# Kernel tuning notes

Hardware: AMD Instinct MI355X
Metric: run time of the kernel (lower is better)

Reference implementation:

```python
import jax, jax.numpy as jnp
import numpy as np

B, T, D = 16, 1024, 768
H = 12
HD = D // H
MLP = 3072


def _layernorm(x, g, b, eps=1e-5):
    mu = jnp.mean(x, axis=-1, keepdims=True)
    var = jnp.var(x, axis=-1, keepdims=True)
    return (x - mu) * jax.lax.rsqrt(var + eps) * g + b


def setup_inputs() -> dict:
    key = jax.random.key(0)
    ks = jax.random.split(key, 12)
    s_d = 1.0 / np.sqrt(D)
    s_m = 1.0 / np.sqrt(MLP)
    return {
        "x": jax.random.normal(ks[0], (B, T, D), dtype=jnp.float32),
        "Wq": jax.random.uniform(ks[1], (D, D), jnp.float32, -s_d, s_d),
        "bq": jnp.zeros((D,), jnp.float32),
        "Wk": jax.random.uniform(ks[2], (D, D), jnp.float32, -s_d, s_d),
        "bk": jnp.zeros((D,), jnp.float32),
        "Wv": jax.random.uniform(ks[3], (D, D), jnp.float32, -s_d, s_d),
        "bv": jnp.zeros((D,), jnp.float32),
        "Wo": jax.random.uniform(ks[4], (D, D), jnp.float32, -s_d, s_d),
        "bo": jnp.zeros((D,), jnp.float32),
        "ln1_g": jnp.ones((D,), jnp.float32),
        "ln1_b": jnp.zeros((D,), jnp.float32),
        "ln2_g": jnp.ones((D,), jnp.float32),
        "ln2_b": jnp.zeros((D,), jnp.float32),
        "W1": jax.random.uniform(ks[5], (D, MLP), jnp.float32, -s_d, s_d),
        "b1": jnp.zeros((MLP,), jnp.float32),
        "W2": jax.random.uniform(ks[6], (MLP, D), jnp.float32, -s_m, s_m),
        "b2": jnp.zeros((D,), jnp.float32),
    }


def reference(x, Wq, bq, Wk, bk, Wv, bv, Wo, bo, ln1_g, ln1_b, ln2_g, ln2_b, W1, b1, W2, b2):
    h = _layernorm(x, ln1_g, ln1_b)
    # QKV projections -> [B, H, T, HD]
    q = (h @ Wq + bq).reshape(B, T, H, HD).transpose(0, 2, 1, 3)
    k = (h @ Wk + bk).reshape(B, T, H, HD).transpose(0, 2, 1, 3)
    v = (h @ Wv + bv).reshape(B, T, H, HD).transpose(0, 2, 1, 3)
    # NOTE: original divides by sqrt(input_dim), not sqrt(head_dim)
    scores = jnp.einsum('bhtf,bhjf->bhtj', q, k) / jnp.sqrt(jnp.float32(D))
    score = jax.nn.softmax(scores, axis=-1)
    attn = jnp.einsum('bhij,bhjf->bihf', score, v)  # [B, T, H, HD]
    attn_out = attn.reshape(B, T, D) @ Wo + bo
    out = attn_out + x
    h2 = _layernorm(out, ln2_g, ln2_b)
    # MLP: Linear -> GELU -> Linear -> GELU (GELU after 2nd linear is in the source)
    m = jax.nn.gelu(h2 @ W1 + b1, approximate=False)
    m = jax.nn.gelu(m @ W2 + b2, approximate=False)
    return m + out
```

## Files before the change

kernel.cpp:

```cpp
#include <hip/hip_runtime.h>
#include <hip/hip_bf16.h>
#include <math.h>

#define D_MODEL 768
#define T_SEQ   1024
#define B_BATCH 16
#define MLP_DIM 3072
#define M_ROWS  (B_BATCH * T_SEQ)

typedef __attribute__((ext_vector_type(8))) __bf16          bf16x8;
typedef __attribute__((ext_vector_type(4))) __bf16          bf16x4;
typedef __attribute__((ext_vector_type(4))) float           f32x4;

__device__ __forceinline__ float bf2f(unsigned short u) {
  union { unsigned int u; float f; } w; w.u = ((unsigned int)u) << 16; return w.f;
}
__device__ __forceinline__ unsigned short f2bf(float f) {
  union { float f; unsigned int u; } w; w.f = f;
  unsigned int r = (w.u + 0x7fffu + ((w.u >> 16) & 1u)) >> 16;
  return (unsigned short)r;
}
__device__ __forceinline__ float gelu_f(float x) {
  return 0.5f * x * (1.0f + erff(x * 0.70710678118654752f));
}
__device__ __forceinline__ void gload16(const void* g, void* l) {
  __builtin_amdgcn_global_load_lds(
      (const __attribute__((address_space(1))) unsigned int*)g,
      (__attribute__((address_space(3))) unsigned int*)l, 16, 0, 0);
}

__global__ void wtr_k(const float* __restrict__ src,
                      unsigned short* __restrict__ dst, int R, int C) {
  __shared__ float t[32][33];
  const int c0 = blockIdx.x * 32, r0 = blockIdx.y * 32;
  const int tx = threadIdx.x, ty = threadIdx.y;
  #pragma unroll
  for (int j = 0; j < 32; j += 8)
    t[ty + j][tx] = src[(size_t)(r0 + ty + j) * C + (c0 + tx)];
  __syncthreads();
  #pragma unroll
  for (int j = 0; j < 32; j += 8)
    dst[(size_t)(c0 + ty + j) * R + (r0 + tx)] = f2bf(t[tx][ty + j]);
}

__global__ void bcat_k(const float* __restrict__ a, const float* __restrict__ b,
                       const float* __restrict__ c, float* __restrict__ o) {
  const int i = blockIdx.x * 256 + threadIdx.x;
  if (i < 768) { o[i] = a[i]; o[i + 768] = b[i]; o[i + 1536] = c[i]; }
}

template<int SRC_F32>
__global__ __launch_bounds__(256) void ln_k(const void* __restrict__ src,
    const float* __restrict__ g, const float* __restrict__ b,
    unsigned short* __restrict__ out) {
  const int row = blockIdx.x, tid = threadIdx.x;
  const size_t base = (size_t)row * D_MODEL;
  float v[3];
  #pragma unroll
  for (int i = 0; i < 3; ++i) {
    const int c = tid + (i << 8);
    v[i] = SRC_F32 ? ((const float*)src)[base + c]
                   : bf2f(((const unsigned short*)src)[base + c]);
  }
  float s  = v[0] + v[1] + v[2];
  float sq = v[0]*v[0] + v[1]*v[1] + v[2]*v[2];
  #pragma unroll
  for (int m = 32; m; m >>= 1) { s += __shfl_xor(s, m); sq += __shfl_xor(sq, m); }
  __shared__ float ps[4], pq[4];
  if ((tid & 63) == 0) { ps[tid >> 6] = s; pq[tid >> 6] = sq; }
  __syncthreads();
  s  = ps[0] + ps[1] + ps[2] + ps[3];
  sq = pq[0] + pq[1] + pq[2] + pq[3];
  const float mu  = s * (1.0f / 768.0f);
  const float var = sq * (1.0f / 768.0f) - mu * mu;
  const float inv = rsqrtf(var + 1e-5f);
  #pragma unroll
  for (int i = 0; i < 3; ++i) {
    const int c = tid + (i << 8);
    out[base + c] = f2bf((v[i] - mu) * inv * g[c] + b[c]);
  }
}

template<int EP>
__global__ __launch_bounds__(512) void gemm_k(
    const unsigned short* __restrict__ Au, const unsigned short* __restrict__ Btu,
    const float* __restrict__ bias, void* __restrict__ outv,
    const void* __restrict__ residv, void* __restrict__ aux,
    int M, int N, int K, int cgrp) {
  __shared__ __align__(16) __bf16 SMEM[2 * 32768];
  const __bf16* A  = (const __bf16*)Au;
  const __bf16* Bt = (const __bf16*)Btu;
  const int tid = threadIdx.x;
  const int lane = tid & 63, w = tid >> 6;
  const int wr = w >> 2, wc = w & 3;
  const int lr = lane & 15, lg = lane >> 4;
  const int gx = gridDim.x, gy = gridDim.y;
  const int bid = blockIdx.y * gx + blockIdx.x;
  const int xcd = bid & 7, idx = bid >> 3;
  const int rpx = gx >> 3;
  const int gsz = rpx * cgrp;
  const int grp = idx / gsz, rem = idx - grp * gsz;
  const int rb = rem / cgrp, cc2 = rem - rb * cgrp + grp * cgrp;
  const int brow = (xcd * rpx + rb) * 256;
  const int bcol = cc2 * 256;

  f32x4 acc[8][4];
  #pragma unroll
  for (int m = 0; m < 8; ++m)
    #pragma unroll
    for (int n = 0; n < 4; ++n) acc[m][n] = (f32x4){0.f, 0.f, 0.f, 0.f};

  const int rrs = lane >> 2;
  const int ccs = (lane & 3) << 3;
  const int csw = ccs ^ ((rrs >> 3) << 4);
  const __bf16* sA[4]; const __bf16* sB[4]; int dA[4], dB[4];
  #pragma unroll
  for (int g = 0; g < 4; ++g) {
    const int s = g * 8 + w;
    const int rsrc = (s >> 1) * 16 + rrs;
    const int csrc = (s & 1) * 32 + csw;
    sA[g] = A  + (size_t)(brow + rsrc) * K + csrc;
    sB[g] = Bt + (size_t)(bcol + rsrc) * K + csrc;
    dA[g] = s * 512;
    dB[g] = 16384 + s * 512;
  }

#define STAGE_(buf_, k0_) do {                                     \
    _Pragma("unroll")                                              \
    for (int g = 0; g < 4; ++g) {                                  \
      gload16(sA[g] + (k0_), &SMEM[(buf_) * 32768 + dA[g]]);       \
      gload16(sB[g] + (k0_), &SMEM[(buf_) * 32768 + dB[g]]);       \
    }                                                              \
  } while (0)

  const int rbase = lr * 32 + ((lg << 3) ^ (((lr >> 3) & 1) << 4));

  STAGE_(0, 0);
  int cur = 0;
  for (int k0 = 0; k0 < K; k0 += 64, cur ^= 1) {
    if (k0 + 64 < K) {
      STAGE_(cur ^ 1, k0 + 64);
      asm volatile("s_waitcnt vmcnt(8)" ::: "memory");
    } else {
      asm volatile("s_waitcnt vmcnt(0)" ::: "memory");
    }
    __builtin_amdgcn_s_barrier();
    __builtin_amdgcn_sched_barrier(0);
    const int bb = cur * 32768;
    bf16x8 bfr[4][2];
    #pragma unroll
    for (int n = 0; n < 4; ++n)
      #pragma unroll
      for (int kk = 0; kk < 2; ++kk)
        bfr[n][kk] = *(const bf16x8*)(&SMEM[bb + 16384 + ((wc*4 + n)*2 + kk)*512 + rbase]);
    __builtin_amdgcn_s_setprio(1);
    #pragma unroll
    for (int mq = 0; mq < 2; ++mq) {
      bf16x8 af[4][2];
      #pragma unroll
      for (int ml = 0; ml < 4; ++ml)
        #pragma unroll
        for (int kk = 0; kk < 2; ++kk)
          af[ml][kk] = *(const bf16x8*)(&SMEM[bb + ((wr*8 + mq*4 + ml)*2 + kk)*512 + rbase]);
      #pragma unroll
      for (int ml = 0; ml < 4; ++ml)
        #pragma unroll
        for (int n = 0; n < 4; ++n) {
          acc[mq*4+ml][n] = __builtin_amdgcn_mfma_f32_16x16x32_bf16(af[ml][0], bfr[n][0], acc[mq*4+ml][n], 0, 0, 0);
          acc[mq*4+ml][n] = __builtin_amdgcn_mfma_f32_16x16x32_bf16(af[ml][1], bfr[n][1], acc[mq*4+ml][n], 0, 0, 0);
        }
    }
    __builtin_amdgcn_s_setprio(0);
    asm volatile("s_waitcnt lgkmcnt(0)" ::: "memory");
    __builtin_amdgcn_sched_barrier(0);
    __builtin_amdgcn_s_barrier();
    __builtin_amdgcn_sched_barrier(0);
  }
#undef STAGE_

  const int seg = (EP == 5) ? (bcol / 768) : 0;
  unsigned short* qkvp = nullptr;
  if (EP == 5)
    qkvp = (seg == 0) ? (unsigned short*)outv
         : (seg == 1) ? (unsigned short*)residv : (unsigned short*)aux;

  if (EP == 5 && seg == 2) {
    #pragma unroll
    for (int n = 0; n < 4; ++n) {
      const int col = bcol + wc*64 + n*16 + lr;
      const float bv = bias[col];
      const int colLv = col - 1536;
      #pragma unroll
      for (int m = 0; m < 8; ++m) {
        const int row0 = brow + wr*128 + m*16 + lg*4;
        #pragma unroll
        for (int r2 = 0; r2 < 4; ++r2) {
          const int gr = row0 + r2;
          qkvp[(((size_t)(gr >> 10) * D_MODEL + colLv) << 10) + (gr & 1023)] =
              f2bf(acc[m][n][r2] + bv);
        }
      }
    }
  } else {
    float* Ep = (float*)SMEM + w * 1280;
    #pragma unroll
    for (int m = 0; m < 8; ++m) {
      #pragma unroll
      for (int n = 0; n < 4; ++n) {
        const int col = bcol + wc*64 + n*16 + lr;
        const float bv = bias[col];
        f32x4 st;
        #pragma unroll
        for (int r2 = 0; r2 < 4; ++r2) {
          float v = acc[m][n][r2] + bv;
          if (EP == 1 || EP == 3) v = gelu_f(v);
          st[r2] = v;
        }
        *(f32x4*)(Ep + (n*16 + lr) * 20 + lg*4) = st;
      }
      #pragma unroll
      for (int i2 = 0; i2 < 2; ++i2) {
        const int rowL = i2*8 + (lane >> 3);
        const int colL = (lane & 7) * 8;
        const int grow = brow + wr*128 + m*16 + rowL;
        const int gcol = bcol + wc*64 + colL;
        float v[8];
        #pragma unroll
        for (int j = 0; j < 8; ++j) v[j] = Ep[(colL + j) * 20 + rowL];
        const size_t o = (size_t)grow * N + gcol;
        if (EP == 3) {
          const bf16x8 rv = *(const bf16x8*)((const __bf16*)residv + o);
          float* op = (float*)outv + o;
          float4 o0, o1;
          o0.x = v[0] + (float)rv[0]; o0.y = v[1] + (float)rv[1];
          o0.z = v[2] + (float)rv[2]; o0.w = v[3] + (float)rv[3];
          o1.x = v[4] + (float)rv[4]; o1.y = v[5] + (float)rv[5];
          o1.z = v[6] + (float)rv[6]; o1.w = v[7] + (float)rv[7];
          *(float4*)op = o0; *(float4*)(op + 4) = o1;
        } else if (EP == 2) {
          const float* rp = (const float*)residv + o;
          const float4 r0 = *(const float4*)rp, r1 = *(const float4*)(rp + 4);
          bf16x8 ov;
          ov[0] = (__bf16)(v[0] + r0.x); ov[1] = (__bf16)(v[1] + r0.y);
          ov[2] = (__bf16)(v[2] + r0.z); ov[3] = (__bf16)(v[3] + r0.w);
          ov[4] = (__bf16)(v[4] + r1.x); ov[5] = (__bf16)(v[5] + r1.y);
          ov[6] = (__bf16)(v[6] + r1.z); ov[7] = (__bf16)(v[7] + r1.w);
          *(bf16x8*)((__bf16*)outv + o) = ov;
        } else if (EP == 5) {
          bf16x8 ov;
          #pragma unroll
          for (int j = 0; j < 8; ++j) ov[j] = (__bf16)v[j];
          *(bf16x8*)((__bf16*)qkvp + (size_t)grow * 768 + (gcol - seg * 768)) = ov;
        } else {
          bf16x8 ov;
          #pragma unroll
          for (int j = 0; j < 8; ++j) ov[j] = (__bf16)v[j];
          *(bf16x8*)((__bf16*)outv + o) = ov;
        }
      }
    }
  }
}

__global__ __launch_bounds__(512) void attn_k(
    const unsigned short* qu, const unsigned short* __restrict__ ku,
    const unsigned short* __restrict__ vtu, unsigned short* attn) {
  __shared__ __align__(16) __bf16 Kl[64][72];
  __shared__ __align__(16) __bf16 Vl[64][72];
  __shared__ __align__(16) __bf16 Pl[8][16][72];
  const __bf16* qg  = (const __bf16*)qu;
  const __bf16* kg  = (const __bf16*)ku;
  const __bf16* vtg = (const __bf16*)vtu;
  const int bid = blockIdx.x;
  const int xcd = bid & 7, idx = bid >> 3;
  const int bh = xcd * 24 + (idx >> 2);
  const int b = bh / 12, h = bh % 12;
  const int q0 = (idx & 3) * 256;
  const int tid = threadIdx.x, lane = tid & 63, w = tid >> 6;
  const int lr = lane & 15, lg = lane >> 4;
  const float scale = 0.03608439182435161f;

  bf16x8 qa[2][2];
  #pragma unroll
  for (int g = 0; g < 2; ++g) {
    const int qrow = b * T_SEQ + q0 + w * 32 + g * 16 + lr;
    const __bf16* qp = qg + (size_t)qrow * D_MODEL + h * 64 + lg * 8;
    qa[g][0] = *(const bf16x8*)(qp);
    qa[g][1] = *(const bf16x8*)(qp + 32);
  }

  const __bf16* kb = kg  + (size_t)b * T_SEQ * D_MODEL + h * 64;
  const __bf16* vb = vtg + ((size_t)b * D_MODEL + h * 64) * T_SEQ;

  f32x4 o[2][4];
  float m_run[2] = {-1e30f, -1e30f}, l_run[2] = {0.f, 0.f};
  #pragma unroll
  for (int g = 0; g < 2; ++g)
    #pragma unroll
    for (int m = 0; m < 4; ++m) o[g][m] = (f32x4){0.f, 0.f, 0.f, 0.f};

  for (int kv0 = 0; kv0 < T_SEQ; kv0 += 64) {
    __syncthreads();
    {
      const int r = tid >> 3, c = (tid & 7) << 3;
      *(bf16x8*)(&Kl[r][c]) = *(const bf16x8*)(kb + (size_t)(kv0 + r) * D_MODEL + c);
      *(bf16x8*)(&Vl[r][c]) = *(const bf16x8*)(vb + (size_t)r * T_SEQ + kv0 + c);
    }
    __syncthreads();

    #pragma unroll
    for (int g = 0; g < 2; ++g) {
      f32x4 s[4];
      __builtin_amdgcn_s_setprio(1);
      #pragma unroll
      for (int m = 0; m < 4; ++m) {
        s[m] = (f32x4){0.f, 0.f, 0.f, 0.f};
        const bf16x8 kf0 = *(const bf16x8*)(&Kl[m*16 + lr][lg*8]);
        const bf16x8 kf1 = *(const bf16x8*)(&Kl[m*16 + lr][32 + lg*8]);
        s[m] = __builtin_amdgcn_mfma_f32_16x16x32_bf16(kf0, qa[g][0], s[m], 0, 0, 0);
        s[m] = __builtin_amdgcn_mfma_f32_16x16x32_bf16(kf1, qa[g][1], s[m], 0, 0, 0);
      }
      __builtin_amdgcn_s_setprio(0);
      float sv[4][4], tm = -1e30f;
      #pragma unroll
      for (int m = 0; m < 4; ++m)
        #pragma unroll
        for (int r = 0; r < 4; ++r) {
          sv[m][r] = s[m][r] * scale;
          tm = fmaxf(tm, sv[m][r]);
        }
      tm = fmaxf(tm, __shfl_xor(tm, 16));
      tm = fmaxf(tm, __shfl_xor(tm, 32));
      const float mn = fmaxf(m_run[g], tm);
      const float sc = __expf(m_run[g] - mn);
      float ts = 0.f;
      bf16x4 pk[4];
      #pragma unroll
      for (int m = 0; m < 4; ++m)
        #pragma unroll
        for (int r = 0; r < 4; ++r) {
          const float pp = __expf(sv[m][r] - mn);
          ts += pp;
          pk[m][r] = (__bf16)pp;
        }
      ts += __shfl_xor(ts, 16);
      ts += __shfl_xor(ts, 32);
      l_run[g] = l_run[g] * sc + ts;
      m_run[g] = mn;
      #pragma unroll
      for (int m = 0; m < 4; ++m)
        #pragma unroll
        for (int r = 0; r < 4; ++r) o[g][m][r] *= sc;
      #pragma unroll
      for (int m = 0; m < 4; ++m)
        *(bf16x4*)(&Pl[w][lr][16*m + 4*lg]) = pk[m];
      const bf16x8 pf0 = *(const bf16x8*)(&Pl[w][lr][lg*8]);
      const bf16x8 pf1 = *(const bf16x8*)(&Pl[w][lr][32 + lg*8]);
      __builtin_amdgcn_s_setprio(1);
      #pragma unroll
      for (int m = 0; m < 4; ++m) {
        const bf16x8 vf0 = *(const bf16x8*)(&Vl[m*16 + lr][lg*8]);
        const bf16x8 vf1 = *(const bf16x8*)(&Vl[m*16 + lr][32 + lg*8]);
        o[g][m] = __builtin_amdgcn_mfma_f32_16x16x32_bf16(vf0, pf0, o[g][m], 0, 0, 0);
        o[g][m] = __builtin_amdgcn_mfma_f32_16x16x32_bf16(vf1, pf1, o[g][m], 0, 0, 0);
      }
      __builtin_amdgcn_s_setprio(0);
    }
  }

  #pragma unroll
  for (int g = 0; g < 2; ++g) {
    const float inv = 1.0f / l_run[g];
    const int qrow = b * T_SEQ + q0 + w * 32 + g * 16 + lr;
    unsigned short* op = attn + (size_t)qrow * D_MODEL + h * 64;
    #pragma unroll
    for (int m = 0; m < 4; ++m) {
      bf16x4 ov;
      #pragma unroll
      for (int r = 0; r < 4; ++r) ov[r] = (__bf16)(o[g][m][r] * inv);
      *(bf16x4*)(op + 16*m + 4*lg) = ov;
    }
  }
}

extern "C" void kernel_launch(void* const* d_in, const int* in_sizes, int n_in,
                              void* d_out, int out_size, void* d_ws, size_t ws_size,
                              hipStream_t stream) {
  const float* x   = (const float*)d_in[0];
  const float* Wq  = (const float*)d_in[1];
  const float* bq  = (const float*)d_in[2];
  const float* Wk  = (const float*)d_in[3];
  const float* bk  = (const float*)d_in[4];
  const float* Wv  = (const float*)d_in[5];
  const float* bv  = (const float*)d_in[6];
  const float* Wo  = (const float*)d_in[7];
  const float* bo  = (const float*)d_in[8];
  const float* g1  = (const float*)d_in[9];
  const float* bt1 = (const float*)d_in[10];
  const float* g2  = (const float*)d_in[11];
  const float* bt2 = (const float*)d_in[12];
  const float* W1  = (const float*)d_in[13];
  const float* bb1 = (const float*)d_in[14];
  const float* W2  = (const float*)d_in[15];
  const float* bb2 = (const float*)d_in[16];

  const size_t SZ = (size_t)M_ROWS * D_MODEL * 2;
  char* wp = (char*)d_ws;
  unsigned short* wqkvT = (unsigned short*)wp; wp += (size_t)2304 * 768 * 2;
  unsigned short* woT   = (unsigned short*)wp; wp += (size_t)768 * 768 * 2;
  unsigned short* w1T   = (unsigned short*)wp; wp += (size_t)768 * 3072 * 2;
  unsigned short* w2T   = (unsigned short*)wp; wp += (size_t)768 * 3072 * 2;
  float*          bqkv  = (float*)wp;          wp += ((size_t)2304 * 4 + 255) & ~(size_t)255;
  unsigned short* kbuf  = (unsigned short*)wp; wp += SZ;
  unsigned short* vtb   = (unsigned short*)wp;
  unsigned short* res2  = kbuf;
  unsigned short* hid   = vtb;
  const size_t avail = ws_size - (size_t)(wp - (char*)d_ws);
  const int nch = (avail >= (size_t)M_ROWS * MLP_DIM * 2) ? 1
                : (avail >= (size_t)(M_ROWS / 2) * MLP_DIM * 2) ? 2 : 4;

  unsigned short* qd = (unsigned short*)d_out;
  unsigned short* h1 = qd + (size_t)M_ROWS * D_MODEL;
  unsigned short* h2 = h1;

  const dim3 tb(32, 8, 1);
  wtr_k<<<dim3(24, 24), tb, 0, stream>>>(Wq, wqkvT, 768, 768);
  wtr_k<<<dim3(24, 24), tb, 0, stream>>>(Wk, wqkvT + (size_t)768 * 768, 768, 768);
  wtr_k<<<dim3(24, 24), tb, 0, stream>>>(Wv, wqkvT + (size_t)1536 * 768, 768, 768);
  wtr_k<<<dim3(24, 24), tb, 0, stream>>>(Wo, woT, 768, 768);
  wtr_k<<<dim3(96, 24), tb, 0, stream>>>(W1, w1T, 768, 3072);
  wtr_k<<<dim3(24, 96), tb, 0, stream>>>(W2, w2T, 3072, 768);
  bcat_k<<<3, 256, 0, stream>>>(bq, bk, bv, bqkv);

  ln_k<1><<<M_ROWS, 256, 0, stream>>>(x, g1, bt1, h1);

  gemm_k<5><<<dim3(64, 9), 512, 0, stream>>>(h1, wqkvT, bqkv, qd, kbuf, vtb,
                                             M_ROWS, 2304, 768, 9);

  attn_k<<<dim3(768), 512, 0, stream>>>(qd, kbuf, vtb, qd);

  gemm_k<2><<<dim3(64, 3), 512, 0, stream>>>(qd, woT, bo, res2, x, nullptr,
                                             M_ROWS, 768, 768, 3);

  ln_k<0><<<M_ROWS, 256, 0, stream>>>(res2, g2, bt2, h2);

  const int CH = M_ROWS / nch;
  for (int c = 0; c < nch; ++c) {
    const size_t ro = (size_t)c * CH;
    gemm_k<1><<<dim3(CH / 256, 12), 512, 0, stream>>>(h2 + ro * 768, w1T, bb1,
        hid, nullptr, nullptr, CH, 3072, 768, 6);
    gemm_k<3><<<dim3(CH / 256, 3), 512, 0, stream>>>(hid, w2T, bb2,
        (float*)d_out + ro * 768, res2 + ro * 768, nullptr, CH, 768, 3072, 3);
  }
}
```

Before: 508.3 us.

## Interleave GEMM prefetch and LDS fragment loads across four MFMA sub-phases

Splits each K-step of the bf16 MFMA GEMM main loop into four quarter-tile compute phases. Each phase is separated by a barrier and issues one quarter of the next tile's global-to-LDS prefetch plus the LDS fragment reads that the following phase needs. The goal is to spread global loads and LDS reads between MFMA bursts instead of front-loading them. The LDS swizzle is also changed to XOR with a 2-bit row-derived value, to spread bank accesses differently. The cost is more barriers per iteration and tighter vmcnt waits.

Result: no change. 500.0 us (-1.6%).

```diff
diff --git a/kernel.cpp b/kernel.cpp
--- a/kernel.cpp
+++ b/kernel.cpp
@@ -94,7 +94,7 @@
   const int lane = tid & 63, w = tid >> 6;
   const int wr = w >> 2, wc = w & 3;
   const int lr = lane & 15, lg = lane >> 4;
-  const int gx = gridDim.x, gy = gridDim.y;
+  const int gx = gridDim.x;
   const int bid = blockIdx.y * gx + blockIdx.x;
   const int xcd = bid & 7, idx = bid >> 3;
   const int rpx = gx >> 3;
@@ -112,7 +112,7 @@
 
   const int rrs = lane >> 2;
   const int ccs = (lane & 3) << 3;
-  const int csw = ccs ^ ((rrs >> 3) << 4);
+  const int csw = ccs ^ ((((lane >> 3) & 3)) << 3);
   const __bf16* sA[4]; const __bf16* sB[4]; int dA[4], dB[4];
   #pragma unroll
   for (int g = 0; g < 4; ++g) {
@@ -125,58 +125,101 @@
     dB[g] = 16384 + s * 512;
   }
 
-#define STAGE_(buf_, k0_) do {                                     \
-    _Pragma("unroll")                                              \
-    for (int g = 0; g < 4; ++g) {                                  \
-      gload16(sA[g] + (k0_), &SMEM[(buf_) * 32768 + dA[g]]);       \
-      gload16(sB[g] + (k0_), &SMEM[(buf_) * 32768 + dB[g]]);       \
-    }                                                              \
+#define STAGE2_(nbb_, k0_, g_) do {                         \
+    gload16(sA[g_] + (k0_), &SMEM[(nbb_) + dA[g_]]);        \
+    gload16(sB[g_] + (k0_), &SMEM[(nbb_) + dB[g_]]);        \
   } while (0)
 
-  const int rbase = lr * 32 + ((lg << 3) ^ (((lr >> 3) & 1) << 4));
-
-  STAGE_(0, 0);
+  const int rbase = lr * 32 + ((lg << 3) ^ (((lr >> 1) & 3) << 3));
+
+  #pragma unroll
+  for (int g = 0; g < 4; ++g) STAGE2_(0, 0, g);
+
   int cur = 0;
   for (int k0 = 0; k0 < K; k0 += 64, cur ^= 1) {
-    if (k0 + 64 < K) {
-      STAGE_(cur ^ 1, k0 + 64);
-      asm volatile("s_waitcnt vmcnt(8)" ::: "memory");
+    const int bb  = cur * 32768;
+    const int nbb = (cur ^ 1) * 32768;
+    const bool pf = (k0 + 64 < K);
+    bf16x8 af0[4][2], af1[4][2], bfr[4][2];
+    if (pf) {
+      STAGE2_(nbb, k0 + 64, 0);
+      asm volatile("s_waitcnt vmcnt(2)" ::: "memory");
     } else {
       asm volatile("s_waitcnt vmcnt(0)" ::: "memory");
     }
     __builtin_amdgcn_s_barrier();
     __builtin_amdgcn_sched_barrier(0);
-    const int bb = cur * 32768;
-    bf16x8 bfr[4][2];
-    #pragma unroll
-    for (int n = 0; n < 4; ++n)
+    #pragma unroll
+    for (int ml = 0; ml < 4; ++ml)
+      #pragma unroll
+      for (int kk = 0; kk < 2; ++kk)
+        af0[ml][kk] = *(const bf16x8*)(&SMEM[bb + ((wr*8 + ml)*2 + kk)*512 + rbase]);
+    #pragma unroll
+    for (int n = 0; n < 2; ++n)
       #pragma unroll
       for (int kk = 0; kk < 2; ++kk)
         bfr[n][kk] = *(const bf16x8*)(&SMEM[bb + 16384 + ((wc*4 + n)*2 + kk)*512 + rbase]);
-    __builtin_amdgcn_s_setprio(1);
-    #pragma unroll
-    for (int mq = 0; mq < 2; ++mq) {
-      bf16x8 af[4][2];
-      #pragma unroll
-      for (int ml = 0; ml < 4; ++ml)
-        #pragma unroll
-        for (int kk = 0; kk < 2; ++kk)
-          af[ml][kk] = *(const bf16x8*)(&SMEM[bb + ((wr*8 + mq*4 + ml)*2 + kk)*512 + rbase]);
-      #pragma unroll
-      for (int ml = 0; ml < 4; ++ml)
-        #pragma unroll
-        for (int n = 0; n < 4; ++n) {
-          acc[mq*4+ml][n] = __builtin_amdgcn_mfma_f32_16x16x32_bf16(af[ml][0], bfr[n][0], acc[mq*4+ml][n], 0, 0, 0);
-          acc[mq*4+ml][n] = __builtin_amdgcn_mfma_f32_16x16x32_bf16(af[ml][1], bfr[n][1], acc[mq*4+ml][n], 0, 0, 0);
-        }
-    }
-    __builtin_amdgcn_s_setprio(0);
     asm volatile("s_waitcnt lgkmcnt(0)" ::: "memory");
     __builtin_amdgcn_sched_barrier(0);
+    __builtin_amdgcn_s_setprio(1);
+    #pragma unroll
+    for (int ml = 0; ml < 4; ++ml)
+      #pragma unroll
+      for (int n = 0; n < 2; ++n) {
+        acc[ml][n] = __builtin_amdgcn_mfma_f32_16x16x32_bf16(af0[ml][0], bfr[n][0], acc[ml][n], 0, 0, 0);
+        acc[ml][n] = __builtin_amdgcn_mfma_f32_16x16x32_bf16(af0[ml][1], bfr[n][1], acc[ml][n], 0, 0, 0);
+      }
+    __builtin_amdgcn_s_setprio(0);
     __builtin_amdgcn_s_barrier();
+    #pragma unroll
+    for (int n = 2; n < 4; ++n)
+      #pragma unroll
+      for (int kk = 0; kk < 2; ++kk)
+        bfr[n][kk] = *(const bf16x8*)(&SMEM[bb + 16384 + ((wc*4 + n)*2 + kk)*512 + rbase]);
+    if (pf) STAGE2_(nbb, k0 + 64, 1);
+    asm volatile("s_waitcnt lgkmcnt(0)" ::: "memory");
     __builtin_amdgcn_sched_barrier(0);
-  }
-#undef STAGE_
+    __builtin_amdgcn_s_setprio(1);
+    #pragma unroll
+    for (int ml = 0; ml < 4; ++ml)
+      #pragma unroll
+      for (int n = 2; n < 4; ++n) {
+        acc[ml][n] = __builtin_amdgcn_mfma_f32_16x16x32_bf16(af0[ml][0], bfr[n][0], acc[ml][n], 0, 0, 0);
+        acc[ml][n] = __builtin_amdgcn_mfma_f32_16x16x32_bf16(af0[ml][1], bfr[n][1], acc[ml][n], 0, 0, 0);
+      }
+    __builtin_amdgcn_s_setprio(0);
+    __builtin_amdgcn_s_barrier();
+    #pragma unroll
+    for (int ml = 0; ml < 4; ++ml)
+      #pragma unroll
+      for (int kk = 0; kk < 2; ++kk)
+        af1[ml][kk] = *(const bf16x8*)(&SMEM[bb + ((wr*8 + 4 + ml)*2 + kk)*512 + rbase]);
+    if (pf) STAGE2_(nbb, k0 + 64, 2);
+    asm volatile("s_waitcnt lgkmcnt(0)" ::: "memory");
+    __builtin_amdgcn_sched_barrier(0);
+    __builtin_amdgcn_s_setprio(1);
+    #pragma unroll
+    for (int ml = 0; ml < 4; ++ml)
+      #pragma unroll
+      for (int n = 0; n < 2; ++n) {
+        acc[4+ml][n] = __builtin_amdgcn_mfma_f32_16x16x32_bf16(af1[ml][0], bfr[n][0], acc[4+ml][n], 0, 0, 0);
+        acc[4+ml][n] = __builtin_amdgcn_mfma_f32_16x16x32_bf16(af1[ml][1], bfr[n][1], acc[4+ml][n], 0, 0, 0);
+      }
+    __builtin_amdgcn_s_setprio(0);
+    __builtin_amdgcn_s_barrier();
+    if (pf) STAGE2_(nbb, k0 + 64, 3);
+    __builtin_amdgcn_s_setprio(1);
+    #pragma unroll
+    for (int ml = 0; ml < 4; ++ml)
+      #pragma unroll
+      for (int n = 2; n < 4; ++n) {
+        acc[4+ml][n] = __builtin_amdgcn_mfma_f32_16x16x32_bf16(af1[ml][0], bfr[n][0], acc[4+ml][n], 0, 0, 0);
+        acc[4+ml][n] = __builtin_amdgcn_mfma_f32_16x16x32_bf16(af1[ml][1], bfr[n][1], acc[4+ml][n], 0, 0, 0);
+      }
+    __builtin_amdgcn_s_setprio(0);
+    __builtin_amdgcn_s_barrier();
+  }
+#undef STAGE2_
 
   const int seg = (EP == 5) ? (bcol / 768) : 0;
   unsigned short* qkvp = nullptr;
```
